# Optimization experiments

Measured on AMD Instinct MI355X. Metric: run time of the kernel, lower is better.

Reference implementation:

```python
import jax, jax.numpy as jnp
import numpy as np

DEFAULT_MASK_VALUE = -0.7 * float(np.finfo(np.float32).max)

B, S, HQ, HKV, D = 2, 2048, 16, 8, 128
CHUNK = 512


def _chunk_causal_mask(seq_len, chunk_size):
    # True where attention allowed: same chunk AND causal within chunk.
    row = jax.lax.broadcasted_iota(jnp.int32, (seq_len, seq_len), 0)
    col = jax.lax.broadcasted_iota(jnp.int32, (seq_len, seq_len), 1)
    return (row // chunk_size == col // chunk_size) & (row >= col)


def _block_mask_indices(bidirectional_mask):
    # [B, L] 0/1 -> segment ids, e.g. [0,1,1,1,0,0,1,1,0,1,0] -> [0,1,1,1,0,0,2,2,0,3,0]
    m = bidirectional_mask.astype(jnp.int32)
    padded = jnp.pad(m, [(0, 0), (1, 0)], constant_values=0)
    boundary = padded[..., 1:] > padded[..., :-1]
    return m * jnp.cumsum(boundary, axis=-1)


def _bidirectional_block_mask(bidirectional_mask):
    idx = _block_mask_indices(bidirectional_mask)  # [B, L]
    return (idx[:, None, :] == idx[:, :, None]) & (idx[:, :, None] > 0)  # [B, L, L]


def setup_inputs() -> dict:
    key = jax.random.key(0)
    kq, kk, kv, kb = jax.random.split(key, 4)
    q = jax.random.normal(kq, (B, S, HQ, D), dtype=jnp.float32)
    k = jax.random.normal(kk, (B, S, HKV, D), dtype=jnp.float32)
    v = jax.random.normal(kv, (B, S, HKV, D), dtype=jnp.float32)
    bidirectional_mask = jax.random.randint(kb, (B, S), 0, 2, dtype=jnp.int32)
    return {"q": q, "k": k, "v": v, "bidirectional_mask": bidirectional_mask,
            "chunk_size": CHUNK}


def reference(q, k, v, bidirectional_mask, chunk_size):
    b, s, hq, d = q.shape
    hkv = k.shape[2]
    group = hq // hkv  # GQA group size
    scale = 1.0 / jnp.sqrt(jnp.asarray(d, q.dtype))

    # [b, s, hkv, group, d]
    qg = q.reshape(b, s, hkv, group, d) * scale
    # logits: [b, hkv, group, q, kv]
    logits = jnp.einsum("bqhgd,bkhd->bhgqk", qg, k)

    # combined mask: chunked-causal OR bidirectional block (image tokens attend
    # bidirectionally within their contiguous block)
    chunk_mask = _chunk_causal_mask(s, chunk_size)                 # [s, s]
    bidir_mask = _bidirectional_block_mask(bidirectional_mask)    # [b, s, s]
    allowed = chunk_mask[None, :, :] | bidir_mask                  # [b, s, s]
    allowed = allowed[:, None, None, :, :]                         # [b, 1, 1, s, s]

    masked = jnp.where(allowed, logits, DEFAULT_MASK_VALUE)
    probs = jax.nn.softmax(masked, axis=-1)

    out = jnp.einsum("bhgqk,bkhd->bqhgd", probs, v)
    return out.reshape(b, s, hq, d)
```

## Files before the change

kernel.cpp:

```cpp
#include <hip/hip_runtime.h>
#include <hip/hip_bf16.h>

#define SLEN 2048
#define BATCH 2
#define NHQ 16
#define NHKV 8
#define DIM 128
#define SEG 512
#define NSEG (SLEN / SEG)
#define KVROW (NHKV * DIM)

#define KTD (64 * 64)
#define VTD (128 * 32)
#define PLSD (16 * 32)

typedef __attribute__((ext_vector_type(8))) short bf16x8;
typedef __attribute__((ext_vector_type(4))) float f32x4;

static __device__ inline short f2bf(float f) {
    __hip_bfloat16 h = __float2bfloat16(f);
    return *reinterpret_cast<short*>(&h);
}
static __device__ inline unsigned pack_bf2(float lo, float hi) {
    unsigned a = (unsigned)(unsigned short)f2bf(lo);
    unsigned b = (unsigned)(unsigned short)f2bf(hi);
    return a | (b << 16);
}
static __device__ inline float fast_exp2(float x) {
#if __has_builtin(__builtin_amdgcn_exp2f)
    return __builtin_amdgcn_exp2f(x);
#else
    return __builtin_exp2f(x);
#endif
}

__global__ void prep_runs(const int* __restrict__ mask,
                          int* __restrict__ rs, int* __restrict__ re) {
    __shared__ int sm[SLEN];
    const int b     = blockIdx.x >> 3;
    const int slice = blockIdx.x & 7;
    const int* mb = mask + b * SLEN;
    for (int i = threadIdx.x; i < SLEN; i += blockDim.x) sm[i] = mb[i];
    __syncthreads();
    const int i = slice * 256 + threadIdx.x;
    int s0 = -1, e0 = -2;
    if (sm[i] == 1) {
        s0 = i; while (s0 > 0 && sm[s0 - 1] == 1) --s0;
        e0 = i; while (e0 < SLEN - 1 && sm[e0 + 1] == 1) ++e0;
    }
    rs[b * SLEN + i] = s0;
    re[b * SLEN + i] = e0;
}

__global__ __launch_bounds__(512, 2) void attn_fwd(
    const float* __restrict__ Q, const float* __restrict__ K,
    const float* __restrict__ V, const int* __restrict__ rs,
    const int* __restrict__ re, const int* __restrict__ csp,
    float* __restrict__ Out)
{
    const int tid  = threadIdx.x;
    const int wid  = tid >> 6;
    const int lane = tid & 63;
    const int quad = lane >> 4;
    const int n    = lane & 15;

    const int bid = blockIdx.x;
    const int xcd = bid & 7;
    const int M   = (bid >> 3) & 7;
    const int G   = (bid >> 6) * 8 + xcd;
    const int seg = G & 3;
    const int h   = (G >> 2) & 7;
    const int b   = G >> 5;
    const int par = M >> 1;
    const int hq  = h * 2 + (M & 1);

    const int rbase = seg * SEG;
    const int r0 = rbase + (4 * wid + par) * 16;

    __shared__ unsigned pool[2 * KTD + 2 * VTD + 8 * PLSD];
    unsigned* ktp = pool;
    unsigned* vtp = pool + 2 * KTD;
    short*    pw  = (short*)(pool + 2 * KTD + 2 * VTD) + wid * (16 * 64);

    const float scale = 0.08838834764831845f * 1.4426950408889634f;
    const int cs = csp[0];

    const int* rsb = rs + b * SLEN;
    const int* reb = re + b * SLEN;

    const int row  = r0 + n;
    const int rsvq = rsb[row];
    const int csrq = (row / cs) * cs;
    int lo_rt, hi_rt;
    {
        const int revq = reb[row];
        int lo = csrq; if (rsvq >= 0 && rsvq < lo) lo = rsvq;
        int hi = row;  if (revq > hi) hi = revq;
        #pragma unroll
        for (int off = 8; off > 0; off >>= 1) {
            lo = min(lo, __shfl_xor(lo, off, 64));
            hi = max(hi, __shfl_xor(hi, off, 64));
        }
        lo_rt = lo; hi_rt = hi;
    }
    const int cshi = ((r0 + 15) / cs) * cs;

    bf16x8 qa[4];
    {
        const float* qp = Q + (((size_t)(b * SLEN + row) * NHQ + hq) * DIM) + quad * 8;
        #pragma unroll
        for (int kb = 0; kb < 4; ++kb) {
            float4 f0 = *(const float4*)(qp + kb * 32);
            float4 f1 = *(const float4*)(qp + kb * 32 + 4);
            bf16x8 a;
            a[0] = f2bf(f0.x * scale); a[1] = f2bf(f0.y * scale);
            a[2] = f2bf(f0.z * scale); a[3] = f2bf(f0.w * scale);
            a[4] = f2bf(f1.x * scale); a[5] = f2bf(f1.y * scale);
            a[6] = f2bf(f1.z * scale); a[7] = f2bf(f1.w * scale);
            qa[kb] = a;
        }
    }

    int lo_blk, hi_blk;
    {
        int* sred = (int*)pool;
        if (lane == 0) { sred[wid * 2] = lo_rt; sred[wid * 2 + 1] = hi_rt; }
        __syncthreads();
        int lo = 0x7fffffff, hi = 0;
        #pragma unroll
        for (int i = 0; i < 8; ++i) {
            lo = min(lo, sred[2 * i]);
            hi = max(hi, sred[2 * i + 1]);
        }
        __syncthreads();
        lo_blk = lo & ~63;
        hi_blk = hi;
    }

    float lrow[4] = {0.f, 0.f, 0.f, 0.f};
    f32x4 o[8];
    #pragma unroll
    for (int nb = 0; nb < 8; ++nb) o[nb] = (f32x4){0.f, 0.f, 0.f, 0.f};

    const float* Kb = K + ((size_t)b * SLEN * NHKV + h) * DIM;
    const float* Vb = V + ((size_t)b * SLEN * NHKV + h) * DIM;

    const int krow = tid >> 3;
    const int kc8  = tid & 7;
    const int vd   = tid & 127;
    const int vg   = tid >> 7;

    float4 kr[4];
    float  vr[16];
    int    rsv_c;

    {
        const float* kp = Kb + (size_t)(lo_blk + krow) * KVROW + kc8 * 16;
        kr[0] = ((const float4*)kp)[0]; kr[1] = ((const float4*)kp)[1];
        kr[2] = ((const float4*)kp)[2]; kr[3] = ((const float4*)kp)[3];
        const float* vp = Vb + (size_t)(lo_blk + vg * 16) * KVROW + vd;
        #pragma unroll
        for (int i = 0; i < 16; ++i) vr[i] = vp[(size_t)i * KVROW];
        rsv_c = rsb[lo_blk + lane];
    }

    const unsigned kx  = (unsigned)((krow & 7) << 2);
    const unsigned vx  = (unsigned)((vd & 7) << 2);
    const unsigned kxr = (unsigned)((n & 7) << 2);

    int bufi = 0;
    for (int k0 = lo_blk; k0 <= hi_blk; k0 += 64, bufi ^= 1) {
        {
            unsigned* kd = ktp + bufi * KTD;
            const unsigned kb0 = (unsigned)(krow * 64 + kc8 * 8);
            *(uint4*)(kd + ((kb0)     ^ kx)) =
                make_uint4(pack_bf2(kr[0].x, kr[0].y), pack_bf2(kr[0].z, kr[0].w),
                           pack_bf2(kr[1].x, kr[1].y), pack_bf2(kr[1].z, kr[1].w));
            *(uint4*)(kd + ((kb0 + 4) ^ kx)) =
                make_uint4(pack_bf2(kr[2].x, kr[2].y), pack_bf2(kr[2].z, kr[2].w),
                           pack_bf2(kr[3].x, kr[3].y), pack_bf2(kr[3].z, kr[3].w));
            unsigned* vdp = vtp + bufi * VTD;
            const unsigned vb0 = (unsigned)(vd * 32 + vg * 8);
            *(uint4*)(vdp + ((vb0)     ^ vx)) =
                make_uint4(pack_bf2(vr[0], vr[1]),  pack_bf2(vr[2], vr[3]),
                           pack_bf2(vr[4], vr[5]),  pack_bf2(vr[6], vr[7]));
            *(uint4*)(vdp + ((vb0 + 4) ^ vx)) =
                make_uint4(pack_bf2(vr[8], vr[9]),  pack_bf2(vr[10], vr[11]),
                           pack_bf2(vr[12], vr[13]), pack_bf2(vr[14], vr[15]));
        }
        __syncthreads();

        int rsv_n = rsv_c;
        if (k0 + 64 <= hi_blk) {
            const int kn0 = k0 + 64;
            const float* kp = Kb + (size_t)(kn0 + krow) * KVROW + kc8 * 16;
            kr[0] = ((const float4*)kp)[0]; kr[1] = ((const float4*)kp)[1];
            kr[2] = ((const float4*)kp)[2]; kr[3] = ((const float4*)kp)[3];
            const float* vp = Vb + (size_t)(kn0 + vg * 16) * KVROW + vd;
            #pragma unroll
            for (int i = 0; i < 16; ++i) vr[i] = vp[(size_t)i * KVROW];
            rsv_n = rsb[kn0 + lane];
        }

        if ((k0 + 63 >= lo_rt) && (k0 <= hi_rt)) {
            const unsigned* ktb = ktp + bufi * KTD;
            const unsigned* vtb = vtp + bufi * VTD;

            f32x4 sfr[4];
            #pragma unroll
            for (int c = 0; c < 4; ++c) sfr[c] = (f32x4){0.f, 0.f, 0.f, 0.f};
            __builtin_amdgcn_s_setprio(1);
            #pragma unroll
            for (int c = 0; c < 4; ++c) {
                #pragma unroll
                for (int kb = 0; kb < 4; ++kb) {
                    const bf16x8 kf = *(const bf16x8*)(ktb +
                        (((unsigned)((c * 16 + n) * 64 + kb * 16 + quad * 4)) ^ kxr));
                    sfr[c] = __builtin_amdgcn_mfma_f32_16x16x32_bf16(qa[kb], kf, sfr[c], 0, 0, 0);
                }
            }
            __builtin_amdgcn_s_setprio(0);

            const bool fullc = (k0 >= cshi) && (k0 + 63 <= r0);
            if (!fullc) {
                int rsr[4], csr_g[4];
                #pragma unroll
                for (int g = 0; g < 4; ++g) {
                    rsr[g]   = __shfl(rsvq, quad * 4 + g, 64);
                    csr_g[g] = __shfl(csrq, quad * 4 + g, 64);
                }
                #pragma unroll
                for (int c = 0; c < 4; ++c) {
                    const int kcl  = k0 + c * 16 + n;
                    const int rskv = __shfl(rsv_c, c * 16 + n, 64);
                    #pragma unroll
                    for (int g = 0; g < 4; ++g) {
                        const int r = r0 + quad * 4 + g;
                        const bool ok = ((kcl >= csr_g[g]) && (kcl <= r)) ||
                                        (rsr[g] >= 0 && rskv == rsr[g]);
                        if (!ok) sfr[c][g] = -3.0e38f;
                    }
                }
            }

            float psum[4] = {0.f, 0.f, 0.f, 0.f};
            #pragma unroll
            for (int c = 0; c < 4; ++c) {
                #pragma unroll
                for (int g = 0; g < 4; ++g) {
                    const float pv = fast_exp2(sfr[c][g]);
                    psum[g] += pv;
                    const int prow = quad * 4 + g;
                    pw[((unsigned)(prow * 64 + c * 16 + n)) ^ ((unsigned)((prow & 7) << 3))] = f2bf(pv);
                }
            }
            #pragma unroll
            for (int g = 0; g < 4; ++g) lrow[g] += psum[g];

            __builtin_amdgcn_s_setprio(1);
            #pragma unroll
            for (int kb2 = 0; kb2 < 2; ++kb2) {
                const bf16x8 pa = *(const bf16x8*)(pw +
                    (((unsigned)(n * 64 + kb2 * 32 + quad * 8)) ^ ((unsigned)((n & 7) << 3))));
                #pragma unroll
                for (int nb = 0; nb < 8; ++nb) {
                    const bf16x8 vf = *(const bf16x8*)(vtb +
                        (((unsigned)((nb * 16 + n) * 32 + kb2 * 16 + quad * 4)) ^ kxr));
                    o[nb] = __builtin_amdgcn_mfma_f32_16x16x32_bf16(pa, vf, o[nb], 0, 0, 0);
                }
            }
            __builtin_amdgcn_s_setprio(0);
        }

        rsv_c = rsv_n;
    }

    #pragma unroll
    for (int g = 0; g < 4; ++g) {
        float l = lrow[g];
        #pragma unroll
        for (int off = 8; off > 0; off >>= 1)
            l += __shfl_xor(l, off, 64);
        const float inv = 1.0f / l;
        const int r = r0 + quad * 4 + g;
        float* op = Out + ((size_t)(b * SLEN + r) * NHQ + hq) * DIM + n;
        #pragma unroll
        for (int nb = 0; nb < 8; ++nb)
            op[nb * 16] = o[nb][g] * inv;
    }
}

extern "C" void kernel_launch(void* const* d_in, const int* in_sizes, int n_in,
                              void* d_out, int out_size, void* d_ws, size_t ws_size,
                              hipStream_t stream) {
    const float* q  = (const float*)d_in[0];
    const float* k  = (const float*)d_in[1];
    const float* v  = (const float*)d_in[2];
    const int*   bm = (const int*)d_in[3];
    const int*   cs = (const int*)d_in[4];
    float* out = (float*)d_out;

    int* rs = (int*)d_ws;
    int* re = rs + BATCH * SLEN;

    hipLaunchKernelGGL(prep_runs, dim3(BATCH * 8), dim3(256), 0, stream, bm, rs, re);
    hipLaunchKernelGGL(attn_fwd, dim3(BATCH * NHQ * NSEG * 4), dim3(512), 0, stream,
                       q, k, v, rs, re, cs, out);
}
```

Measured before the change: 145.7 us.

## Pre-convert K/V to bf16 in a prep kernel and stream tiles via global_load_lds

Adds a conversion kernel that casts K to bf16 in a per-head contiguous layout and writes V transposed in bf16, fused with the existing mask run computation. The attention kernel then loads pre-swizzled K/V tiles directly into LDS with global_load_lds, double-buffered, instead of loading fp32 through registers, packing and storing to LDS each iteration. This halves global bytes per tile and removes per-iteration conversion work. The cost is an extra pass over K/V and a workspace round trip, plus a sync moved to the end of the loop.

```diff
diff --git a/kernel.cpp b/kernel.cpp
--- a/kernel.cpp
+++ b/kernel.cpp
@@ -34,27 +34,81 @@
 #endif
 }
 
-__global__ void prep_runs(const int* __restrict__ mask,
-                          int* __restrict__ rs, int* __restrict__ re) {
-    __shared__ int sm[SLEN];
-    const int b     = blockIdx.x >> 3;
-    const int slice = blockIdx.x & 7;
-    const int* mb = mask + b * SLEN;
-    for (int i = threadIdx.x; i < SLEN; i += blockDim.x) sm[i] = mb[i];
+#define GLDS(g, l) __builtin_amdgcn_global_load_lds( \
+    (const __attribute__((address_space(1))) void*)(g), \
+    (__attribute__((address_space(3))) void*)(l), 16, 0, 0)
+
+__global__ __launch_bounds__(256) void conv_kv(
+    const float* __restrict__ K, const float* __restrict__ V,
+    unsigned short* __restrict__ Kb, unsigned short* __restrict__ Vt,
+    const int* __restrict__ mask, int* __restrict__ rs, int* __restrict__ re)
+{
+    __shared__ float vt_s[64 * 132];
+    __shared__ int   sm[SLEN];
+    const int blk = blockIdx.x;
+    const int NCONV = BATCH * NHKV * (SLEN / 64);
+
+    if (blk >= NCONV) {
+        const int idx = blk - NCONV;
+        const int b = idx >> 3, slice = idx & 7;
+        const int* mb = mask + b * SLEN;
+        for (int i = threadIdx.x; i < SLEN; i += 256) sm[i] = mb[i];
+        __syncthreads();
+        const int i = slice * 256 + threadIdx.x;
+        int s0 = -1, e0 = -2;
+        if (sm[i] == 1) {
+            s0 = i; while (s0 > 0 && sm[s0 - 1] == 1) --s0;
+            e0 = i; while (e0 < SLEN - 1 && sm[e0 + 1] == 1) ++e0;
+        }
+        rs[b * SLEN + i] = s0;
+        re[b * SLEN + i] = e0;
+        return;
+    }
+
+    const int st = blk & 31;
+    const int h  = (blk >> 5) & 7;
+    const int b  = blk >> 8;
+    const int s0 = st * 64;
+    const int sl = threadIdx.x >> 2;
+    const int dq = (threadIdx.x & 3) * 32;
+
+    {
+        const float* ksrc = K + (((size_t)(b * SLEN + s0 + sl) * NHKV + h) * DIM) + dq;
+        unsigned short* kdst = Kb + (((size_t)(b * NHKV + h) * SLEN) + s0 + sl) * DIM + dq;
+        #pragma unroll
+        for (int i = 0; i < 4; ++i) {
+            float4 a = ((const float4*)ksrc)[2 * i];
+            float4 c = ((const float4*)ksrc)[2 * i + 1];
+            ((uint4*)kdst)[i] = make_uint4(pack_bf2(a.x, a.y), pack_bf2(a.z, a.w),
+                                           pack_bf2(c.x, c.y), pack_bf2(c.z, c.w));
+        }
+    }
+
+    {
+        const float* vsrc = V + (((size_t)(b * SLEN + s0 + sl) * NHKV + h) * DIM) + dq;
+        float4* ld = (float4*)&vt_s[sl * 132 + dq];
+        #pragma unroll
+        for (int i = 0; i < 8; ++i) ld[i] = ((const float4*)vsrc)[i];
+    }
     __syncthreads();
-    const int i = slice * 256 + threadIdx.x;
-    int s0 = -1, e0 = -2;
-    if (sm[i] == 1) {
-        s0 = i; while (s0 > 0 && sm[s0 - 1] == 1) --s0;
-        e0 = i; while (e0 < SLEN - 1 && sm[e0 + 1] == 1) ++e0;
-    }
-    rs[b * SLEN + i] = s0;
-    re[b * SLEN + i] = e0;
+    #pragma unroll
+    for (int pass = 0; pass < 2; ++pass) {
+        const int dl = (threadIdx.x >> 2) + pass * 64;
+        const int sw = (threadIdx.x & 3) * 16;
+        unsigned pk[8];
+        #pragma unroll
+        for (int m = 0; m < 8; ++m)
+            pk[m] = pack_bf2(vt_s[(sw + 2 * m) * 132 + dl],
+                             vt_s[(sw + 2 * m + 1) * 132 + dl]);
+        unsigned short* dst = Vt + (((size_t)(b * NHKV + h) * DIM) + dl) * SLEN + s0 + sw;
+        ((uint4*)dst)[0] = make_uint4(pk[0], pk[1], pk[2], pk[3]);
+        ((uint4*)dst)[1] = make_uint4(pk[4], pk[5], pk[6], pk[7]);
+    }
 }
 
 __global__ __launch_bounds__(512, 2) void attn_fwd(
-    const float* __restrict__ Q, const float* __restrict__ K,
-    const float* __restrict__ V, const int* __restrict__ rs,
+    const float* __restrict__ Q, const unsigned short* __restrict__ KbP,
+    const unsigned short* __restrict__ VtP, const int* __restrict__ rs,
     const int* __restrict__ re, const int* __restrict__ csp,
     float* __restrict__ Out)
 {
@@ -78,9 +132,7 @@
     const int r0 = rbase + (4 * wid + par) * 16;
 
     __shared__ unsigned pool[2 * KTD + 2 * VTD + 8 * PLSD];
-    unsigned* ktp = pool;
-    unsigned* vtp = pool + 2 * KTD;
-    short*    pw  = (short*)(pool + 2 * KTD + 2 * VTD) + wid * (16 * 64);
+    short* pw = (short*)(pool + 2 * KTD + 2 * VTD) + wid * (16 * 64);
 
     const float scale = 0.08838834764831845f * 1.4426950408889634f;
     const int cs = csp[0];
@@ -142,69 +194,57 @@
     #pragma unroll
     for (int nb = 0; nb < 8; ++nb) o[nb] = (f32x4){0.f, 0.f, 0.f, 0.f};
 
-    const float* Kb = K + ((size_t)b * SLEN * NHKV + h) * DIM;
-    const float* Vb = V + ((size_t)b * SLEN * NHKV + h) * DIM;
-
-    const int krow = tid >> 3;
-    const int kc8  = tid & 7;
-    const int vd   = tid & 127;
-    const int vg   = tid >> 7;
-
-    float4 kr[4];
-    float  vr[16];
-    int    rsv_c;
-
-    {
-        const float* kp = Kb + (size_t)(lo_blk + krow) * KVROW + kc8 * 16;
-        kr[0] = ((const float4*)kp)[0]; kr[1] = ((const float4*)kp)[1];
-        kr[2] = ((const float4*)kp)[2]; kr[3] = ((const float4*)kp)[3];
-        const float* vp = Vb + (size_t)(lo_blk + vg * 16) * KVROW + vd;
-        #pragma unroll
-        for (int i = 0; i < 16; ++i) vr[i] = vp[(size_t)i * KVROW];
-        rsv_c = rsb[lo_blk + lane];
-    }
-
-    const unsigned kx  = (unsigned)((krow & 7) << 2);
-    const unsigned vx  = (unsigned)((vd & 7) << 2);
+    const unsigned short* KbB = KbP + (size_t)(b * NHKV + h) * SLEN * DIM;
+    const unsigned short* VtB = VtP + (size_t)(b * NHKV + h) * DIM * SLEN;
+    int ks_off[2], vs_off[2];
+    unsigned kl_off[2], vl_off[2];
+    #pragma unroll
+    for (int q2 = 0; q2 < 2; ++q2) {
+        const int B = q2 * 512 + tid;
+        { const int r = B >> 4, j = B & 15;
+          const int sj = (j & 8) | ((j & 7) ^ (r & 7));
+          ks_off[q2] = r * DIM + sj * 8;  kl_off[q2] = (unsigned)B * 16; }
+        { const int r = B >> 3, j = B & 7;
+          const int sj = j ^ (r & 7);
+          vs_off[q2] = r * SLEN + sj * 8; vl_off[q2] = (unsigned)B * 16; }
+    }
+
     const unsigned kxr = (unsigned)((n & 7) << 2);
+
+    {
+        const unsigned short* kbt = KbB + (size_t)lo_blk * DIM;
+        const unsigned short* vtt = VtB + lo_blk;
+        char* kl = (char*)pool;
+        char* vl = (char*)pool + 32768;
+        #pragma unroll
+        for (int q2 = 0; q2 < 2; ++q2) {
+            GLDS(kbt + ks_off[q2], kl + kl_off[q2]);
+            GLDS(vtt + vs_off[q2], vl + vl_off[q2]);
+        }
+    }
+    int rsv_c = rsb[lo_blk + lane];
+    __syncthreads();
 
     int bufi = 0;
     for (int k0 = lo_blk; k0 <= hi_blk; k0 += 64, bufi ^= 1) {
-        {
-            unsigned* kd = ktp + bufi * KTD;
-            const unsigned kb0 = (unsigned)(krow * 64 + kc8 * 8);
-            *(uint4*)(kd + ((kb0)     ^ kx)) =
-                make_uint4(pack_bf2(kr[0].x, kr[0].y), pack_bf2(kr[0].z, kr[0].w),
-                           pack_bf2(kr[1].x, kr[1].y), pack_bf2(kr[1].z, kr[1].w));
-            *(uint4*)(kd + ((kb0 + 4) ^ kx)) =
-                make_uint4(pack_bf2(kr[2].x, kr[2].y), pack_bf2(kr[2].z, kr[2].w),
-                           pack_bf2(kr[3].x, kr[3].y), pack_bf2(kr[3].z, kr[3].w));
-            unsigned* vdp = vtp + bufi * VTD;
-            const unsigned vb0 = (unsigned)(vd * 32 + vg * 8);
-            *(uint4*)(vdp + ((vb0)     ^ vx)) =
-                make_uint4(pack_bf2(vr[0], vr[1]),  pack_bf2(vr[2], vr[3]),
-                           pack_bf2(vr[4], vr[5]),  pack_bf2(vr[6], vr[7]));
-            *(uint4*)(vdp + ((vb0 + 4) ^ vx)) =
-                make_uint4(pack_bf2(vr[8], vr[9]),  pack_bf2(vr[10], vr[11]),
-                           pack_bf2(vr[12], vr[13]), pack_bf2(vr[14], vr[15]));
-        }
-        __syncthreads();
-
         int rsv_n = rsv_c;
         if (k0 + 64 <= hi_blk) {
             const int kn0 = k0 + 64;
-            const float* kp = Kb + (size_t)(kn0 + krow) * KVROW + kc8 * 16;
-            kr[0] = ((const float4*)kp)[0]; kr[1] = ((const float4*)kp)[1];
-            kr[2] = ((const float4*)kp)[2]; kr[3] = ((const float4*)kp)[3];
-            const float* vp = Vb + (size_t)(kn0 + vg * 16) * KVROW + vd;
-            #pragma unroll
-            for (int i = 0; i < 16; ++i) vr[i] = vp[(size_t)i * KVROW];
+            const unsigned short* kbt = KbB + (size_t)kn0 * DIM;
+            const unsigned short* vtt = VtB + kn0;
+            char* kl = (char*)pool + (bufi ^ 1) * 16384;
+            char* vl = (char*)pool + 32768 + (bufi ^ 1) * 16384;
+            #pragma unroll
+            for (int q2 = 0; q2 < 2; ++q2) {
+                GLDS(kbt + ks_off[q2], kl + kl_off[q2]);
+                GLDS(vtt + vs_off[q2], vl + vl_off[q2]);
+            }
             rsv_n = rsb[kn0 + lane];
         }
 
         if ((k0 + 63 >= lo_rt) && (k0 <= hi_rt)) {
-            const unsigned* ktb = ktp + bufi * KTD;
-            const unsigned* vtb = vtp + bufi * VTD;
+            const unsigned* ktb = pool + bufi * KTD;
+            const unsigned* vtb = pool + 2 * KTD + bufi * VTD;
 
             f32x4 sfr[4];
             #pragma unroll
@@ -272,6 +312,7 @@
             __builtin_amdgcn_s_setprio(0);
         }
 
+        __syncthreads();
         rsv_c = rsv_n;
     }
 
@@ -302,8 +343,11 @@
 
     int* rs = (int*)d_ws;
     int* re = rs + BATCH * SLEN;
-
-    hipLaunchKernelGGL(prep_runs, dim3(BATCH * 8), dim3(256), 0, stream, bm, rs, re);
+    unsigned short* Kb = (unsigned short*)((char*)d_ws + 32768);
+    unsigned short* Vt = Kb + (size_t)BATCH * NHKV * SLEN * DIM;
+
+    hipLaunchKernelGGL(conv_kv, dim3(BATCH * NHKV * (SLEN / 64) + BATCH * 8), dim3(256),
+                       0, stream, k, v, Kb, Vt, bm, rs, re);
     hipLaunchKernelGGL(attn_fwd, dim3(BATCH * NHQ * NSEG * 4), dim3(512), 0, stream,
-                       q, k, v, rs, re, cs, out);
-}
+                       q, Kb, Vt, rs, re, cs, out);
+}
```

After: 150.5 us. +3.3%, slower.
